# Optimization experiments

Hardware: AMD Instinct MI355X
Metric: run time of the kernel (lower is better)

## Reference

```python
import jax, jax.numpy as jnp
import numpy as np

B, WIN, D, H, O, P = 512, 128, 256, 512, 64, 64  # batch, window, input_size, hidden, output, plength


def setup_inputs() -> dict:
    key = jax.random.key(0)
    ks = jax.random.split(key, 14)
    s = 0.05
    return {
        "x": jax.random.normal(ks[0], (B, WIN, D), jnp.float32),
        # AdditiveScore params: V (v_d,), W (v_d, 2H), U (v_d, k_d) with v_d = k_d = D
        "V": jax.random.normal(ks[1], (D,), jnp.float32) * s,
        "W": jax.random.normal(ks[2], (D, 2 * H), jnp.float32) * s,
        "U": jax.random.normal(ks[3], (D, D), jnp.float32) * s,
        # LSTM (1 layer, gate order i,f,g,o): input dim D+O
        "W_ih": jax.random.normal(ks[4], (4 * H, D + O), jnp.float32) * s,
        "W_hh": jax.random.normal(ks[5], (4 * H, H), jnp.float32) * s,
        "b_ih": jax.random.normal(ks[6], (4 * H,), jnp.float32) * s,
        "b_hh": jax.random.normal(ks[7], (4 * H,), jnp.float32) * s,
        # dense: hidden -> output
        "Wd": jax.random.normal(ks[8], (O, H), jnp.float32) * s,
        "bd": jax.random.normal(ks[9], (O,), jnp.float32) * s,
        # context_s / context_c: input -> hidden
        "Ws": jax.random.normal(ks[10], (H, D), jnp.float32) * s,
        "bs": jax.random.normal(ks[11], (H,), jnp.float32) * s,
        "Wc": jax.random.normal(ks[12], (H, D), jnp.float32) * s,
        "bc": jax.random.normal(ks[13], (H,), jnp.float32) * s,
    }


def reference(x, V, W, U, W_ih, W_hh, b_ih, b_hh, Wd, bd, Ws, bs, Wc, bc):
    # initial decoder state from last encoder step
    h0 = jnp.tanh(x[:, -1] @ Ws.T + bs)            # (B, H)
    c0 = jax.nn.sigmoid(x[:, -1] @ Wc.T + bc)      # (B, H)
    y0 = jnp.zeros((x.shape[0], bd.shape[0]), x.dtype)
    # U*k is constant across decode steps: precompute once
    Uk = jnp.einsum('vd,bwd->bvw', U, x)

    def step(carry, _):
        h, c, y = carry
        q = jnp.concatenate([h, c], axis=-1)        # (B, 2H)
        Wq = q @ W.T                                # (B, D)
        # e = V^T tanh(Wq + Uk); softmax over window
        score = jnp.einsum('v,bvw->bw', V, jnp.tanh(Wq[:, :, None] + Uk))
        att = jax.nn.softmax(score, axis=-1)
        ctx = jnp.einsum('bw,bwd->bd', att, x)      # (B, D)
        inp = jnp.concatenate([y, ctx], axis=-1)    # (B, O+D)
        gates = inp @ W_ih.T + h @ W_hh.T + b_ih + b_hh
        i_, f_, g_, o_ = jnp.split(gates, 4, axis=-1)
        c_new = jax.nn.sigmoid(f_) * c + jax.nn.sigmoid(i_) * jnp.tanh(g_)
        h_new = jax.nn.sigmoid(o_) * jnp.tanh(c_new)
        y_new = h_new @ Wd.T + bd                   # (B, O)
        return (h_new, c_new, y_new), (y_new, att)

    _, (ys, atts) = jax.lax.scan(step, (h0, c0, y0), None, length=P)
    predict_y = jnp.transpose(ys, (1, 0, 2))        # (B, P, O)
    weight = jnp.transpose(atts, (1, 0, 2))
    return predict_y, weight
```

## Files before the change

kernel.cpp:

```cpp
#include <hip/hip_runtime.h>
#include <hip/hip_bf16.h>

#define B_   512
#define WIN_ 128
#define D_   256
#define H_   512
#define O_   64
#define P_   64
#define K2H  1024
#define KG   832
#define NG   2048
#define NSLN 320

typedef __attribute__((ext_vector_type(8))) short bf16x8;
typedef __attribute__((ext_vector_type(4))) float f32x4;
using bf16 = __hip_bfloat16;

__device__ __forceinline__ float fast_tanh(float x){
    float e = __expf(2.f * x);
    return 1.f - __fdividef(2.f, e + 1.f);
}
__device__ __forceinline__ float fast_sig(float x){
    return __fdividef(1.f, 1.f + __expf(-x));
}
__device__ __forceinline__ float b_lo(unsigned int u){ return __uint_as_float(u << 16); }
__device__ __forceinline__ float b_hi(unsigned int u){ return __uint_as_float(u & 0xffff0000u); }
__device__ __forceinline__ short f2bs(float v){
    return (short)__builtin_bit_cast(unsigned short, __float2bfloat16(v));
}
__device__ __forceinline__ unsigned int pack2(float a, float b){
    unsigned short sa = __builtin_bit_cast(unsigned short, __float2bfloat16(a));
    unsigned short sb = __builtin_bit_cast(unsigned short, __float2bfloat16(b));
    return (unsigned int)sa | ((unsigned int)sb << 16);
}

__global__ void k_prep(const float* __restrict__ x, const float* __restrict__ W,
                       const float* __restrict__ U, const float* __restrict__ W_ih,
                       const float* __restrict__ W_hh, const float* __restrict__ b_ih,
                       const float* __restrict__ b_hh, const float* __restrict__ Wd,
                       const float* __restrict__ Ws, const float* __restrict__ Wc,
                       bf16* __restrict__ x_bf, bf16* __restrict__ Wcomb,
                       bf16* __restrict__ Wsl, bf16* __restrict__ U_bf,
                       bf16* __restrict__ Wsc, float* __restrict__ bsum)
{
    const long NXv = (long)B_ * WIN_ * D_ / 8;
    const long NWC = (long)NG * KG;
    const long NSL = (long)8 * NSLN * 128;
    const long NU  = (long)D_ * D_;
    const long NWS = (long)K2H * D_;
    const long NB  = NG;
    const long total = NXv + NWC + NSL + NU + NWS + NB;
    for (long i = (long)blockIdx.x * blockDim.x + threadIdx.x; i < total;
         i += (long)gridDim.x * blockDim.x) {
        long j = i;
        if (j < NXv) {
            const float4* xp = (const float4*)x + j * 2;
            float4 a = xp[0], b = xp[1];
            bf16x8 v;
            v[0] = f2bs(a.x); v[1] = f2bs(a.y); v[2] = f2bs(a.z); v[3] = f2bs(a.w);
            v[4] = f2bs(b.x); v[5] = f2bs(b.y); v[6] = f2bs(b.z); v[7] = f2bs(b.w);
            *(bf16x8*)((short*)x_bf + j * 8) = v;
            continue;
        }
        j -= NXv;
        if (j < NWC) {
            long n = j / KG, k = j % KG;
            float v = (k < 320) ? W_ih[n * 320 + k] : W_hh[n * 512 + (k - 320)];
            Wcomb[j] = __float2bfloat16(v); continue;
        }
        j -= NWC;
        if (j < NSL) {
            long by = j / (NSLN * 128);
            long rem = j % (NSLN * 128);
            long n = rem / 128, k = rem % 128;
            float v;
            if (n < 256) v = (k < 64) ? W[n * K2H + by * 64 + k]
                                      : W[n * K2H + 512 + by * 64 + (k - 64)];
            else         v = (k < 64) ? Wd[(n - 256) * H_ + by * 64 + k] : 0.f;
            Wsl[j] = __float2bfloat16(v); continue;
        }
        j -= NSL;
        if (j < NU) { U_bf[j] = __float2bfloat16(U[j]); continue; }
        j -= NU;
        if (j < NWS) {
            long n = j / D_, k = j % D_;
            float v = (n < 512) ? Ws[n * D_ + k] : Wc[(n - 512) * D_ + k];
            Wsc[j] = __float2bfloat16(v); continue;
        }
        j -= NWS;
        bsum[j] = b_ih[j] + b_hh[j];
    }
}

__global__ void __launch_bounds__(256) k_init2(const bf16* __restrict__ x_bf,
                       const bf16* __restrict__ Wsc, const float* __restrict__ bs,
                       const float* __restrict__ bc, bf16* __restrict__ q_buf,
                       bf16* __restrict__ A0, float* __restrict__ c_f32)
{
    int wave = threadIdx.x >> 6, lane = threadIdx.x & 63;
    int m0 = blockIdx.x * 16;
    int n0 = blockIdx.y * 64 + wave * 16;
    int r = lane & 15, ko = (lane >> 4) * 8, rj = (lane >> 4) * 4;
    const short* xp = (const short*)x_bf;
    const short* wp = (const short*)Wsc;
    f32x4 acc = {};
    #pragma unroll
    for (int k0 = 0; k0 < D_; k0 += 32) {
        bf16x8 a  = *(const bf16x8*)(xp + (long)(m0 + r) * (WIN_ * D_) + 127 * D_ + k0 + ko);
        bf16x8 bb = *(const bf16x8*)(wp + (long)(n0 + r) * D_ + k0 + ko);
        acc = __builtin_amdgcn_mfma_f32_16x16x32_bf16(a, bb, acc, 0, 0, 0);
    }
    int n = n0 + r;
    if (n0 < 512) {
        float bias = bs[n];
        #pragma unroll
        for (int j = 0; j < 4; ++j) {
            int b = m0 + rj + j;
            float hv = fast_tanh(acc[j] + bias);
            bf16 hb = __float2bfloat16(hv);
            q_buf[(long)b * K2H + n]   = hb;
            A0[(long)b * KG + 320 + n] = hb;
        }
    } else {
        float bias = bc[n - 512];
        #pragma unroll
        for (int j = 0; j < 4; ++j) {
            int b = m0 + rj + j;
            float cv = fast_sig(acc[j] + bias);
            q_buf[(long)b * K2H + n]        = __float2bfloat16(cv);
            c_f32[(long)b * H_ + (n - 512)] = cv;
        }
    }
}

__global__ void __launch_bounds__(256) k_uk(const bf16* __restrict__ U_bf,
                    const bf16* __restrict__ x_bf, bf16* __restrict__ Uk)
{
    __shared__ __align__(16) short xs[64][264];
    int b  = blockIdx.y;
    int v0 = (blockIdx.x >> 1) * 64;
    int w0 = (blockIdx.x & 1) * 64;
    {
        const short* xg = (const short*)x_bf + (long)b * (WIN_ * D_) + (long)w0 * D_;
        int row = threadIdx.x >> 2, c4 = (threadIdx.x & 3) * 8;
        #pragma unroll
        for (int i = 0; i < 8; ++i)
            *(bf16x8*)(&xs[row][c4 + i * 32]) = *(const bf16x8*)(xg + (long)row * D_ + c4 + i * 32);
    }
    __syncthreads();
    int lane = threadIdx.x & 63;
    int wave = threadIdx.x >> 6;
    int r  = lane & 15;
    int ko = (lane >> 4) * 8;
    const short* Up = (const short*)U_bf + (long)(v0 + wave * 16 + r) * D_;
    f32x4 acc[4] = {};
    #pragma unroll 2
    for (int k0 = 0; k0 < D_; k0 += 32) {
        bf16x8 a = *(const bf16x8*)(Up + k0 + ko);
        #pragma unroll
        for (int f = 0; f < 4; ++f) {
            bf16x8 bb = *(const bf16x8*)(&xs[f * 16 + r][k0 + ko]);
            acc[f] = __builtin_amdgcn_mfma_f32_16x16x32_bf16(a, bb, acc[f], 0, 0, 0);
        }
    }
    bf16* up = Uk + (long)b * (D_ * WIN_);
    int vbase = v0 + wave * 16 + (lane >> 4) * 4;
    #pragma unroll
    for (int f = 0; f < 4; ++f) {
        int w = w0 + f * 16 + r;
        #pragma unroll
        for (int j = 0; j < 4; ++j)
            up[(long)(vbase + j) * WIN_ + w] = __float2bfloat16(acc[f][j]);
    }
}

__global__ void __launch_bounds__(256) k_slab0(const bf16* __restrict__ q_buf,
                     const bf16* __restrict__ Wsl, float* __restrict__ slab)
{
    int bx = blockIdx.x, by = blockIdx.y;
    int wave = threadIdx.x >> 6, lane = threadIdx.x & 63;
    int r = lane & 15, ko = (lane >> 4) * 8, rj = (lane >> 4) * 4;
    int m0 = bx * 16;
    const short* qp = (const short*)q_buf;
    const short* wp = (const short*)Wsl + (long)by * NSLN * 128;
    #pragma unroll
    for (int i = 0; i < 5; ++i) {
        int n0 = (wave * 5 + i) * 16;
        f32x4 acc = {};
        #pragma unroll
        for (int k0 = 0; k0 < 128; k0 += 32) {
            long koff = (k0 < 64) ? (by * 64 + k0) : (512 + by * 64 + (k0 - 64));
            bf16x8 a  = *(const bf16x8*)(qp + (long)(m0 + r) * K2H + koff + ko);
            bf16x8 bb = *(const bf16x8*)(wp + (long)(n0 + r) * 128 + k0 + ko);
            acc = __builtin_amdgcn_mfma_f32_16x16x32_bf16(a, bb, acc, 0, 0, 0);
        }
        int n = n0 + r;
        #pragma unroll
        for (int j = 0; j < 4; ++j)
            slab[((long)by * B_ + m0 + rj + j) * NSLN + n] = acc[j];
    }
}

__global__ void __launch_bounds__(256) k_att(
    const bf16* __restrict__ x_bf, const bf16* __restrict__ Uk,
    const float* __restrict__ slab, const float* __restrict__ V,
    const float* __restrict__ bd, bf16* __restrict__ A_cur,
    float* __restrict__ out_y, float* __restrict__ out_w, int s)
{
    __shared__ float v_s[D_];
    __shared__ float wq_s[D_];
    __shared__ float part[16][136];
    __shared__ float att_s[WIN_];
    __shared__ float cpart[8][264];
    __shared__ float redw[4];

    const int b = blockIdx.x;
    const int t = threadIdx.x;
    const int lane = t & 63;

    v_s[t] = V[t];
    {
        float wsum = 0.f;
        #pragma unroll
        for (int by = 0; by < 8; ++by)
            wsum += slab[((long)by * B_ + b) * NSLN + t];
        wq_s[t] = wsum;
    }
    if (t < O_) {
        if (s > 0) {
            float yv = bd[t];
            #pragma unroll
            for (int by = 0; by < 8; ++by)
                yv += slab[((long)by * B_ + b) * NSLN + 256 + t];
            out_y[((long)b * P_ + (s - 1)) * O_ + t] = yv;
            A_cur[(long)b * KG + t] = __float2bfloat16(yv);
        } else {
            A_cur[(long)b * KG + t] = __float2bfloat16(0.f);
        }
    }
    __syncthreads();

    {
        const int w16 = t & 15, vg = t >> 4;
        const uint4* ukp = (const uint4*)((const short*)Uk + (long)b * (D_ * WIN_));
        float scv[8] = {0.f,0.f,0.f,0.f,0.f,0.f,0.f,0.f};
        #pragma unroll
        for (int half = 0; half < 2; ++half) {
            uint4 u[8];
            #pragma unroll
            for (int i = 0; i < 8; ++i)
                u[i] = ukp[(long)(vg * 16 + half * 8 + i) * 16 + w16];
            #pragma unroll
            for (int i = 0; i < 8; ++i) {
                int v = vg * 16 + half * 8 + i;
                float wqv = wq_s[v], vv = v_s[v];
                scv[0] += vv * fast_tanh(wqv + b_lo(u[i].x));
                scv[1] += vv * fast_tanh(wqv + b_hi(u[i].x));
                scv[2] += vv * fast_tanh(wqv + b_lo(u[i].y));
                scv[3] += vv * fast_tanh(wqv + b_hi(u[i].y));
                scv[4] += vv * fast_tanh(wqv + b_lo(u[i].z));
                scv[5] += vv * fast_tanh(wqv + b_hi(u[i].z));
                scv[6] += vv * fast_tanh(wqv + b_lo(u[i].w));
                scv[7] += vv * fast_tanh(wqv + b_hi(u[i].w));
            }
        }
        #pragma unroll
        for (int j = 0; j < 8; ++j) part[vg][w16 * 8 + j] = scv[j];
    }
    __syncthreads();

    float e = 0.f, scw = 0.f;
    if (t < WIN_) {
        #pragma unroll
        for (int q = 0; q < 16; ++q) scw += part[q][t];
        float m = scw;
        #pragma unroll
        for (int off = 32; off > 0; off >>= 1) m = fmaxf(m, __shfl_xor(m, off));
        if (lane == 0) redw[t >> 6] = m;
    }
    __syncthreads();
    if (t < WIN_) {
        float m = fmaxf(redw[0], redw[1]);
        e = __expf(scw - m);
        float l = e;
        #pragma unroll
        for (int off = 32; off > 0; off >>= 1) l += __shfl_xor(l, off);
        if (lane == 0) redw[2 + (t >> 6)] = l;
    }
    __syncthreads();
    if (t < WIN_) {
        float a = __fdividef(e, redw[2] + redw[3]);
        att_s[t] = a;
        out_w[((long)b * P_ + s) * WIN_ + t] = a;
    }
    __syncthreads();

    {
        const int dg = t & 31, wg = t >> 5;
        const uint4* xp = (const uint4*)((const short*)x_bf + (long)b * (WIN_ * D_));
        float cacc[8] = {0.f,0.f,0.f,0.f,0.f,0.f,0.f,0.f};
        #pragma unroll
        for (int half = 0; half < 2; ++half) {
            uint4 u[8];
            #pragma unroll
            for (int i = 0; i < 8; ++i)
                u[i] = xp[(long)(wg * 16 + half * 8 + i) * 32 + dg];
            #pragma unroll
            for (int i = 0; i < 8; ++i) {
                float a = att_s[wg * 16 + half * 8 + i];
                cacc[0] += a * b_lo(u[i].x);
                cacc[1] += a * b_hi(u[i].x);
                cacc[2] += a * b_lo(u[i].y);
                cacc[3] += a * b_hi(u[i].y);
                cacc[4] += a * b_lo(u[i].z);
                cacc[5] += a * b_hi(u[i].z);
                cacc[6] += a * b_lo(u[i].w);
                cacc[7] += a * b_hi(u[i].w);
            }
        }
        #pragma unroll
        for (int j = 0; j < 8; ++j) cpart[wg][dg * 8 + j] = cacc[j];
    }
    __syncthreads();
    if (t < 128) {
        int d = t * 2;
        float f0 = 0.f, f1 = 0.f;
        #pragma unroll
        for (int q = 0; q < 8; ++q) { f0 += cpart[q][d]; f1 += cpart[q][d + 1]; }
        *(unsigned int*)(A_cur + (long)b * KG + O_ + d) = pack2(f0, f1);
    }
}

__global__ void __launch_bounds__(256) k_gates(const bf16* __restrict__ A_in,
                     const bf16* __restrict__ Wcomb, const bf16* __restrict__ Wsl,
                     const float* __restrict__ bsum, float* __restrict__ c_f32,
                     bf16* __restrict__ A_out, float* __restrict__ slab)
{
    __shared__ short lhc[16][136];
    int bx = blockIdx.x, by = blockIdx.y;
    int wave = threadIdx.x >> 6, lane = threadIdx.x & 63;
    int r = lane & 15, ko = (lane >> 4) * 8, rj = (lane >> 4) * 4;
    int m0 = bx * 16;
    int jw = by * 64 + wave * 16;
    const short* ap = (const short*)A_in;
    const short* wp = (const short*)Wcomb;
    f32x4 acc[4] = {};
    long arow = (long)(m0 + r) * KG;
    #pragma unroll 2
    for (int k0 = 0; k0 < KG; k0 += 32) {
        bf16x8 a = *(const bf16x8*)(ap + arow + k0 + ko);
        #pragma unroll
        for (int g = 0; g < 4; ++g) {
            bf16x8 bb = *(const bf16x8*)(wp + (long)(g * H_ + jw + r) * KG + k0 + ko);
            acc[g] = __builtin_amdgcn_mfma_f32_16x16x32_bf16(a, bb, acc[g], 0, 0, 0);
        }
    }
    int jj = jw + r;
    float bi = bsum[jj], bf_ = bsum[H_ + jj], bg = bsum[2*H_ + jj], bo = bsum[3*H_ + jj];
    #pragma unroll
    for (int j = 0; j < 4; ++j) {
        int b = m0 + rj + j;
        float iv = acc[0][j] + bi;
        float fv = acc[1][j] + bf_;
        float gv = acc[2][j] + bg;
        float ov = acc[3][j] + bo;
        float c_old = c_f32[(long)b * H_ + jj];
        float cn = fast_sig(fv) * c_old + fast_sig(iv) * fast_tanh(gv);
        float hn = fast_sig(ov) * fast_tanh(cn);
        c_f32[(long)b * H_ + jj] = cn;
        short hb = f2bs(hn);
        A_out[(long)b * KG + 320 + jj] = __builtin_bit_cast(bf16, (unsigned short)hb);
        lhc[rj + j][wave * 16 + r]      = hb;
        lhc[rj + j][64 + wave * 16 + r] = f2bs(cn);
    }
    __syncthreads();
    const short* wsl = (const short*)Wsl + (long)by * NSLN * 128;
    #pragma unroll
    for (int i = 0; i < 5; ++i) {
        int n0 = (wave * 5 + i) * 16;
        f32x4 pac = {};
        #pragma unroll
        for (int k0 = 0; k0 < 128; k0 += 32) {
            bf16x8 a  = *(const bf16x8*)(&lhc[r][k0 + ko]);
            bf16x8 bb = *(const bf16x8*)(wsl + (long)(n0 + r) * 128 + k0 + ko);
            pac = __builtin_amdgcn_mfma_f32_16x16x32_bf16(a, bb, pac, 0, 0, 0);
        }
        int n = n0 + r;
        #pragma unroll
        for (int j = 0; j < 4; ++j)
            slab[((long)by * B_ + m0 + rj + j) * NSLN + n] = pac[j];
    }
}

__global__ void __launch_bounds__(256) k_yfin(const float* __restrict__ slab,
                     const float* __restrict__ bd, float* __restrict__ out_y)
{
    int b = blockIdx.x * 4 + (threadIdx.x >> 6);
    int o = threadIdx.x & 63;
    float yv = bd[o];
    #pragma unroll
    for (int by = 0; by < 8; ++by)
        yv += slab[((long)by * B_ + b) * NSLN + 256 + o];
    out_y[((long)b * P_ + 63) * O_ + o] = yv;
}

extern "C" void kernel_launch(void* const* d_in, const int* in_sizes, int n_in,
                              void* d_out, int out_size, void* d_ws, size_t ws_size,
                              hipStream_t stream)
{
    const float* x    = (const float*)d_in[0];
    const float* V    = (const float*)d_in[1];
    const float* W    = (const float*)d_in[2];
    const float* U    = (const float*)d_in[3];
    const float* W_ih = (const float*)d_in[4];
    const float* W_hh = (const float*)d_in[5];
    const float* b_ih = (const float*)d_in[6];
    const float* b_hh = (const float*)d_in[7];
    const float* Wd   = (const float*)d_in[8];
    const float* bd   = (const float*)d_in[9];
    const float* Ws   = (const float*)d_in[10];
    const float* bs   = (const float*)d_in[11];
    const float* Wc   = (const float*)d_in[12];
    const float* bc   = (const float*)d_in[13];

    float* out_y = (float*)d_out;
    float* out_w = (float*)d_out + (long)B_ * P_ * O_;

    char* p = (char*)d_ws;
    auto alloc = [&](size_t bytes) { char* r = p; p += (bytes + 255) & ~(size_t)255; return r; };
    bf16*  x_bf  = (bf16*) alloc((size_t)B_ * WIN_ * D_ * 2);
    bf16*  Uk    = (bf16*) alloc((size_t)B_ * D_ * WIN_ * 2);
    bf16*  q_buf = (bf16*) alloc((size_t)B_ * K2H * 2);
    bf16*  A0    = (bf16*) alloc((size_t)B_ * KG * 2);
    bf16*  A1    = (bf16*) alloc((size_t)B_ * KG * 2);
    float* c_f32 = (float*)alloc((size_t)B_ * H_ * 4);
    float* slab  = (float*)alloc((size_t)8 * B_ * NSLN * 4);
    bf16*  Wcomb = (bf16*) alloc((size_t)NG * KG * 2);
    bf16*  Wsl   = (bf16*) alloc((size_t)8 * NSLN * 128 * 2);
    bf16*  U_bf  = (bf16*) alloc((size_t)D_ * D_ * 2);
    bf16*  Wsc   = (bf16*) alloc((size_t)K2H * D_ * 2);
    float* bsum  = (float*)alloc((size_t)NG * 4);
    bf16*  Abuf[2] = { A0, A1 };

    k_prep<<<8192, 256, 0, stream>>>(x, W, U, W_ih, W_hh, b_ih, b_hh, Wd, Ws, Wc,
                                     x_bf, Wcomb, Wsl, U_bf, Wsc, bsum);
    k_init2<<<dim3(32, 16), 256, 0, stream>>>(x_bf, Wsc, bs, bc, q_buf, A0, c_f32);
    k_uk<<<dim3(8, 512), 256, 0, stream>>>(U_bf, x_bf, Uk);
    k_slab0<<<dim3(32, 8), 256, 0, stream>>>(q_buf, Wsl, slab);

    for (int s = 0; s < P_; ++s) {
        k_att<<<512, 256, 0, stream>>>(x_bf, Uk, slab, V, bd,
                                       Abuf[s & 1], out_y, out_w, s);
        k_gates<<<dim3(32, 8), 256, 0, stream>>>(Abuf[s & 1], Wcomb, Wsl, bsum,
                                                 c_f32, Abuf[(s + 1) & 1], slab);
    }
    k_yfin<<<128, 256, 0, stream>>>(slab, bd, out_y);
}
```

Measured before the change: 2.577 ms.

## Fuse attention and LSTM gate kernels into one per-step kernel with flag sync

Merges the per-step gate GEMM kernel and the attention kernel into a single launch. The first 256 blocks compute the previous step's gates and slab partials, then signal per-row-tile atomic counters. Each attention block spins on its tile's counter before it reads the slab. The final y output is folded into an extra 65th launch, and the flags are zeroed in the prep kernel. This halves the number of launches and lets attention for finished row tiles overlap with gates still in progress. The cost is a cross-block spin-wait that assumes co-residency, plus a guard-break timeout that could silently produce wrong data.

```diff
diff --git a/kernel.cpp b/kernel.cpp
--- a/kernel.cpp
+++ b/kernel.cpp
@@ -41,8 +41,10 @@
                        const float* __restrict__ Ws, const float* __restrict__ Wc,
                        bf16* __restrict__ x_bf, bf16* __restrict__ Wcomb,
                        bf16* __restrict__ Wsl, bf16* __restrict__ U_bf,
-                       bf16* __restrict__ Wsc, float* __restrict__ bsum)
-{
+                       bf16* __restrict__ Wsc, float* __restrict__ bsum,
+                       unsigned int* __restrict__ tile_flag)
+{
+    if (blockIdx.x == 0 && threadIdx.x < 32) tile_flag[threadIdx.x] = 0u;
     const long NXv = (long)B_ * WIN_ * D_ / 8;
     const long NWC = (long)NG * KG;
     const long NSL = (long)8 * NSLN * 128;
@@ -201,11 +203,14 @@
     }
 }
 
-__global__ void __launch_bounds__(256) k_att(
+__global__ void __launch_bounds__(256) k_step(
     const bf16* __restrict__ x_bf, const bf16* __restrict__ Uk,
-    const float* __restrict__ slab, const float* __restrict__ V,
-    const float* __restrict__ bd, bf16* __restrict__ A_cur,
-    float* __restrict__ out_y, float* __restrict__ out_w, int s)
+    float* __restrict__ slab, const float* __restrict__ V,
+    const float* __restrict__ bd, bf16* __restrict__ A0, bf16* __restrict__ A1,
+    float* __restrict__ out_y, float* __restrict__ out_w,
+    const bf16* __restrict__ Wcomb, const bf16* __restrict__ Wsl,
+    const float* __restrict__ bsum, float* __restrict__ c_f32,
+    unsigned int* __restrict__ tile_flag, int s)
 {
     __shared__ float v_s[D_];
     __shared__ float wq_s[D_];
@@ -213,10 +218,104 @@
     __shared__ float att_s[WIN_];
     __shared__ float cpart[8][264];
     __shared__ float redw[4];
-
-    const int b = blockIdx.x;
+    __shared__ short lhc[16][136];
+
+    const int g = blockIdx.x;
     const int t = threadIdx.x;
     const int lane = t & 63;
+    const int wave = t >> 6;
+    const int r = lane & 15, ko = (lane >> 4) * 8, rj = (lane >> 4) * 4;
+
+    bf16* A_cur        = (s & 1) ? A1 : A0;
+    const bf16* A_prev = (s & 1) ? A0 : A1;
+
+    if (g < 256 && s > 0) {
+        int bx = g & 31, by = g >> 5;
+        int m0 = bx * 16;
+        int jw = by * 64 + wave * 16;
+        const short* ap = (const short*)A_prev;
+        const short* wp = (const short*)Wcomb;
+        f32x4 acc[4] = {};
+        long arow = (long)(m0 + r) * KG;
+        #pragma unroll 2
+        for (int k0 = 0; k0 < KG; k0 += 32) {
+            bf16x8 a = *(const bf16x8*)(ap + arow + k0 + ko);
+            #pragma unroll
+            for (int gq = 0; gq < 4; ++gq) {
+                bf16x8 bb = *(const bf16x8*)(wp + (long)(gq * H_ + jw + r) * KG + k0 + ko);
+                acc[gq] = __builtin_amdgcn_mfma_f32_16x16x32_bf16(a, bb, acc[gq], 0, 0, 0);
+            }
+        }
+        int jj = jw + r;
+        float bi = bsum[jj], bf_ = bsum[H_ + jj];
+        float bg2 = bsum[2 * H_ + jj], bo = bsum[3 * H_ + jj];
+        #pragma unroll
+        for (int j = 0; j < 4; ++j) {
+            int bb2 = m0 + rj + j;
+            float iv = acc[0][j] + bi;
+            float fv = acc[1][j] + bf_;
+            float gv = acc[2][j] + bg2;
+            float ov = acc[3][j] + bo;
+            float c_old = c_f32[(long)bb2 * H_ + jj];
+            float cn = fast_sig(fv) * c_old + fast_sig(iv) * fast_tanh(gv);
+            float hn = fast_sig(ov) * fast_tanh(cn);
+            c_f32[(long)bb2 * H_ + jj] = cn;
+            short hb = f2bs(hn);
+            A_cur[(long)bb2 * KG + 320 + jj] = __builtin_bit_cast(bf16, (unsigned short)hb);
+            lhc[rj + j][wave * 16 + r]      = hb;
+            lhc[rj + j][64 + wave * 16 + r] = f2bs(cn);
+        }
+        __syncthreads();
+        const short* wsl = (const short*)Wsl + (long)by * NSLN * 128;
+        #pragma unroll
+        for (int i = 0; i < 5; ++i) {
+            int n0 = (wave * 5 + i) * 16;
+            f32x4 pac = {};
+            #pragma unroll
+            for (int k0 = 0; k0 < 128; k0 += 32) {
+                bf16x8 a  = *(const bf16x8*)(&lhc[r][k0 + ko]);
+                bf16x8 bb = *(const bf16x8*)(wsl + (long)(n0 + r) * 128 + k0 + ko);
+                pac = __builtin_amdgcn_mfma_f32_16x16x32_bf16(a, bb, pac, 0, 0, 0);
+            }
+            int n = n0 + r;
+            #pragma unroll
+            for (int j = 0; j < 4; ++j)
+                slab[((long)by * B_ + m0 + rj + j) * NSLN + n] = pac[j];
+        }
+        __syncthreads();
+        if (t == 0) {
+            __threadfence();
+            __hip_atomic_fetch_add(&tile_flag[bx], 1u, __ATOMIC_RELAXED,
+                                   __HIP_MEMORY_SCOPE_AGENT);
+        }
+    }
+
+    const int b = g;
+
+    if (s > 0) {
+        if (t == 0) {
+            const unsigned int target = 8u * (unsigned int)s;
+            int guard = 0;
+            while (__hip_atomic_load(&tile_flag[b >> 4], __ATOMIC_RELAXED,
+                                     __HIP_MEMORY_SCOPE_AGENT) < target) {
+                __builtin_amdgcn_s_sleep(8);
+                if (++guard > (1 << 20)) break;
+            }
+            __threadfence();
+        }
+        __syncthreads();
+    }
+
+    if (s == P_) {
+        if (t < O_) {
+            float yv = bd[t];
+            #pragma unroll
+            for (int by = 0; by < 8; ++by)
+                yv += slab[((long)by * B_ + b) * NSLN + 256 + t];
+            out_y[((long)b * P_ + 63) * O_ + t] = yv;
+        }
+        return;
+    }
 
     v_s[t] = V[t];
     {
@@ -329,79 +428,6 @@
         for (int q = 0; q < 8; ++q) { f0 += cpart[q][d]; f1 += cpart[q][d + 1]; }
         *(unsigned int*)(A_cur + (long)b * KG + O_ + d) = pack2(f0, f1);
     }
-}
-
-__global__ void __launch_bounds__(256) k_gates(const bf16* __restrict__ A_in,
-                     const bf16* __restrict__ Wcomb, const bf16* __restrict__ Wsl,
-                     const float* __restrict__ bsum, float* __restrict__ c_f32,
-                     bf16* __restrict__ A_out, float* __restrict__ slab)
-{
-    __shared__ short lhc[16][136];
-    int bx = blockIdx.x, by = blockIdx.y;
-    int wave = threadIdx.x >> 6, lane = threadIdx.x & 63;
-    int r = lane & 15, ko = (lane >> 4) * 8, rj = (lane >> 4) * 4;
-    int m0 = bx * 16;
-    int jw = by * 64 + wave * 16;
-    const short* ap = (const short*)A_in;
-    const short* wp = (const short*)Wcomb;
-    f32x4 acc[4] = {};
-    long arow = (long)(m0 + r) * KG;
-    #pragma unroll 2
-    for (int k0 = 0; k0 < KG; k0 += 32) {
-        bf16x8 a = *(const bf16x8*)(ap + arow + k0 + ko);
-        #pragma unroll
-        for (int g = 0; g < 4; ++g) {
-            bf16x8 bb = *(const bf16x8*)(wp + (long)(g * H_ + jw + r) * KG + k0 + ko);
-            acc[g] = __builtin_amdgcn_mfma_f32_16x16x32_bf16(a, bb, acc[g], 0, 0, 0);
-        }
-    }
-    int jj = jw + r;
-    float bi = bsum[jj], bf_ = bsum[H_ + jj], bg = bsum[2*H_ + jj], bo = bsum[3*H_ + jj];
-    #pragma unroll
-    for (int j = 0; j < 4; ++j) {
-        int b = m0 + rj + j;
-        float iv = acc[0][j] + bi;
-        float fv = acc[1][j] + bf_;
-        float gv = acc[2][j] + bg;
-        float ov = acc[3][j] + bo;
-        float c_old = c_f32[(long)b * H_ + jj];
-        float cn = fast_sig(fv) * c_old + fast_sig(iv) * fast_tanh(gv);
-        float hn = fast_sig(ov) * fast_tanh(cn);
-        c_f32[(long)b * H_ + jj] = cn;
-        short hb = f2bs(hn);
-        A_out[(long)b * KG + 320 + jj] = __builtin_bit_cast(bf16, (unsigned short)hb);
-        lhc[rj + j][wave * 16 + r]      = hb;
-        lhc[rj + j][64 + wave * 16 + r] = f2bs(cn);
-    }
-    __syncthreads();
-    const short* wsl = (const short*)Wsl + (long)by * NSLN * 128;
-    #pragma unroll
-    for (int i = 0; i < 5; ++i) {
-        int n0 = (wave * 5 + i) * 16;
-        f32x4 pac = {};
-        #pragma unroll
-        for (int k0 = 0; k0 < 128; k0 += 32) {
-            bf16x8 a  = *(const bf16x8*)(&lhc[r][k0 + ko]);
-            bf16x8 bb = *(const bf16x8*)(wsl + (long)(n0 + r) * 128 + k0 + ko);
-            pac = __builtin_amdgcn_mfma_f32_16x16x32_bf16(a, bb, pac, 0, 0, 0);
-        }
-        int n = n0 + r;
-        #pragma unroll
-        for (int j = 0; j < 4; ++j)
-            slab[((long)by * B_ + m0 + rj + j) * NSLN + n] = pac[j];
-    }
-}
-
-__global__ void __launch_bounds__(256) k_yfin(const float* __restrict__ slab,
-                     const float* __restrict__ bd, float* __restrict__ out_y)
-{
-    int b = blockIdx.x * 4 + (threadIdx.x >> 6);
-    int o = threadIdx.x & 63;
-    float yv = bd[o];
-    #pragma unroll
-    for (int by = 0; by < 8; ++by)
-        yv += slab[((long)by * B_ + b) * NSLN + 256 + o];
-    out_y[((long)b * P_ + 63) * O_ + o] = yv;
 }
 
 extern "C" void kernel_launch(void* const* d_in, const int* in_sizes, int n_in,
@@ -440,19 +466,17 @@
     bf16*  U_bf  = (bf16*) alloc((size_t)D_ * D_ * 2);
     bf16*  Wsc   = (bf16*) alloc((size_t)K2H * D_ * 2);
     float* bsum  = (float*)alloc((size_t)NG * 4);
-    bf16*  Abuf[2] = { A0, A1 };
+    unsigned int* tile_flag = (unsigned int*)alloc(256);
 
     k_prep<<<8192, 256, 0, stream>>>(x, W, U, W_ih, W_hh, b_ih, b_hh, Wd, Ws, Wc,
-                                     x_bf, Wcomb, Wsl, U_bf, Wsc, bsum);
+                                     x_bf, Wcomb, Wsl, U_bf, Wsc, bsum, tile_flag);
     k_init2<<<dim3(32, 16), 256, 0, stream>>>(x_bf, Wsc, bs, bc, q_buf, A0, c_f32);
     k_uk<<<dim3(8, 512), 256, 0, stream>>>(U_bf, x_bf, Uk);
     k_slab0<<<dim3(32, 8), 256, 0, stream>>>(q_buf, Wsl, slab);
 
-    for (int s = 0; s < P_; ++s) {
-        k_att<<<512, 256, 0, stream>>>(x_bf, Uk, slab, V, bd,
-                                       Abuf[s & 1], out_y, out_w, s);
-        k_gates<<<dim3(32, 8), 256, 0, stream>>>(Abuf[s & 1], Wcomb, Wsl, bsum,
-                                                 c_f32, Abuf[(s + 1) & 1], slab);
-    }
-    k_yfin<<<128, 256, 0, stream>>>(slab, bd, out_y);
-}
+    for (int s = 0; s <= P_; ++s) {
+        k_step<<<512, 256, 0, stream>>>(x_bf, Uk, slab, V, bd, A0, A1,
+                                        out_y, out_w, Wcomb, Wsl, bsum,
+                                        c_f32, tile_flag, s);
+    }
+}
```

New measurement: 4.330 ms. 68.0% more time.
